# Optimization experiments

Measured on AMD Instinct MI355X. Metric: run time of the kernel, lower is better.

The kernel has to match this reference:

```python
import jax, jax.numpy as jnp
import numpy as np

B, S, D_IN, D_OUT = 4, 2048, 1024, 1024

def setup_inputs() -> dict:
    key = jax.random.key(0)
    k1, k2, k3, k4 = jax.random.split(key, 4)
    s = 0.02
    return {
        "X": jax.random.normal(k1, (B, S, D_IN), dtype=jnp.float32),
        "Wq": jax.random.normal(k2, (D_OUT, D_IN), dtype=jnp.float32) * s,
        "Wk": jax.random.normal(k3, (D_OUT, D_IN), dtype=jnp.float32) * s,
        "Wv": jax.random.normal(k4, (D_OUT, D_IN), dtype=jnp.float32) * s,
    }

def reference(X, Wq, Wk, Wv):
    # nn.Linear: y = x @ W.T (no bias)
    q = jnp.einsum('bsd,ed->bse', X, Wq)  # [B,S,D_OUT]
    k = jnp.einsum('bsd,ed->bse', X, Wk)
    v = jnp.einsum('bsd,ed->bse', X, Wv)
    scores = jnp.einsum('bqe,bke->bqk', q, k)  # [B,S,S]
    n = X.shape[1]
    causal = jnp.triu(jnp.ones((n, n), dtype=bool), k=1)
    scores = jnp.where(causal[None], -jnp.inf, scores)
    scale = 1.0 / jnp.sqrt(jnp.asarray(k.shape[-1], dtype=scores.dtype))
    attn = jax.nn.softmax(scores * scale, axis=-1)
    return jnp.einsum('bqk,bke->bqe', attn, v)
```

## Files before the change

kernel.cpp:

```cpp
#include <hip/hip_runtime.h>
#include <cstdint>


typedef __attribute__((ext_vector_type(8))) __bf16 bf16x8;
typedef __attribute__((ext_vector_type(4))) float f32x4;

#define BK 64

__device__ __forceinline__ unsigned short f2bf(float f) {
  union { float f; unsigned u; } v; v.f = f;
  unsigned r = v.u + 0x7fffu + ((v.u >> 16) & 1u);
  return (unsigned short)(r >> 16);
}

__device__ __forceinline__ void gload_lds16(const void* g, void* l) {
  __builtin_amdgcn_global_load_lds(
      (const __attribute__((address_space(1))) void*)g,
      (__attribute__((address_space(3))) void*)l, 16, 0, 0);
}

__global__ __launch_bounds__(256)
void cvt_all(const float* __restrict__ X, const float* __restrict__ Wq,
             const float* __restrict__ Wk, const float* __restrict__ Wv,
             unsigned short* __restrict__ Xbf, unsigned short* __restrict__ Wall,
             float* __restrict__ L) {
  const int bid = blockIdx.x;
  if (bid >= 11264) {
    float4* p = (float4*)(L + (size_t)(bid - 11264) * 2048);
    p[threadIdx.x] = (float4){0.f, 0.f, 0.f, 0.f};
    p[threadIdx.x + 256] = (float4){0.f, 0.f, 0.f, 0.f};
    return;
  }
  const float* src;
  unsigned short* dst;
  int i;
  if (bid < 8192) {
    src = X; dst = Xbf; i = bid * 256 + threadIdx.x;
  } else {
    const int m = bid - 8192;
    const int sel = m >> 10;
    src = (sel == 0) ? Wq : (sel == 1) ? Wk : Wv;
    dst = Wall + (size_t)sel * 1048576;
    i = (m & 1023) * 256 + threadIdx.x;
  }
  float4 v = ((const float4*)src)[i];
  ushort4 o;
  o.x = f2bf(v.x); o.y = f2bf(v.y); o.z = f2bf(v.z); o.w = f2bf(v.w);
  ((ushort4*)dst)[i] = o;
}

__global__ __launch_bounds__(256, 3)
void gemm_qkv(const unsigned short* __restrict__ A,
              const unsigned short* __restrict__ Bm,
              unsigned short* __restrict__ Qb,
              unsigned short* __restrict__ Kb,
              unsigned short* __restrict__ Vt,
              int bx0)
{
  const int NX = gridDim.x;
  const int lin = blockIdx.y * NX + blockIdx.x;
  const int chunk = (NX * 64) >> 3;
  const int swz = (lin & 7) * chunk + (lin >> 3);
  const int bx = swz % NX + bx0, by = swz / NX;

  __shared__ __align__(16) unsigned short As[128 * BK];
  __shared__ __align__(16) unsigned short Bs[128 * BK];

  const int tid = threadIdx.x;
  const int wave = tid >> 6, lane = tid & 63;
  const int wr = wave >> 1, wc = wave & 1;
  const int quad = lane >> 4, l16 = lane & 15;

  const unsigned rsub = wave * 8 + (lane >> 3);
  const unsigned csb = (unsigned)(((lane & 7) ^ ((lane >> 3) & 7)) * 16);

  unsigned offA[4], offB[4];
  #pragma unroll
  for (int s = 0; s < 4; ++s) {
    offA[s] = ((unsigned)(by * 128 + s * 32 + rsub) * 1024u) * 2u + csb;
    offB[s] = ((unsigned)(bx * 128 + s * 32 + rsub) * 1024u) * 2u + csb;
  }
  const char* Abase = (const char*)A;
  const char* Bbase = (const char*)Bm;

  f32x4 acc[4][4];
  #pragma unroll
  for (int i = 0; i < 4; ++i)
    #pragma unroll
    for (int j = 0; j < 4; ++j)
      acc[i][j] = (f32x4){0.f, 0.f, 0.f, 0.f};

  const int pq = (quad ^ (l16 & 7)) * 8;
  const int aOff = (wr * 64 + l16) * BK + pq;
  const int bOff = (wc * 64 + l16) * BK + pq;

  for (int k0 = 0; k0 < 1024; k0 += BK) {
    const unsigned kb = (unsigned)k0 * 2u;
    #pragma unroll
    for (int s = 0; s < 4; ++s) {
      gload_lds16(Abase + kb + offA[s], As + s * 2048 + wave * 512);
      gload_lds16(Bbase + kb + offB[s], Bs + s * 2048 + wave * 512);
    }
    __syncthreads();
    #pragma unroll
    for (int h = 0; h < 2; ++h) {
      const int hx = h * 32;
      bf16x8 af[4], bfr[4];
      #pragma unroll
      for (int i = 0; i < 4; ++i)
        af[i] = *(const bf16x8*)(As + ((aOff + i * 16 * BK) ^ hx));
      #pragma unroll
      for (int j = 0; j < 4; ++j)
        bfr[j] = *(const bf16x8*)(Bs + ((bOff + j * 16 * BK) ^ hx));
      #pragma unroll
      for (int i = 0; i < 4; ++i)
        #pragma unroll
        for (int j = 0; j < 4; ++j)
          acc[i][j] = __builtin_amdgcn_mfma_f32_16x16x32_bf16(af[i], bfr[j], acc[i][j], 0, 0, 0);
    }
    __syncthreads();
  }

  const int row0 = by * 128 + wr * 64 + quad * 4;
  const int col0 = bx * 128 + wc * 64 + l16;
  if (bx < 16) {
    unsigned short* C = (bx < 8) ? Qb : Kb;
    const int col = (bx < 8) ? col0 : col0 - 1024;
    #pragma unroll
    for (int i = 0; i < 4; ++i)
      #pragma unroll
      for (int r = 0; r < 4; ++r) {
        const size_t rr = (size_t)(row0 + i * 16 + r) * 1024;
        #pragma unroll
        for (int j = 0; j < 4; ++j)
          C[rr + col + j * 16] = f2bf(acc[i][j][r]);
      }
  } else {
    const int b = row0 >> 11;
    const int s0 = row0 & 2047;
    unsigned short* Vb = Vt + (size_t)b * 2097152;
    #pragma unroll
    for (int j = 0; j < 4; ++j) {
      const size_t ee = (size_t)(col0 - 2048 + j * 16) * 2048;
      #pragma unroll
      for (int i = 0; i < 4; ++i) {
        ushort4 o;
        o.x = f2bf(acc[i][j][0]); o.y = f2bf(acc[i][j][1]);
        o.z = f2bf(acc[i][j][2]); o.w = f2bf(acc[i][j][3]);
        *(ushort4*)(Vb + ee + s0 + i * 16) = o;
      }
    }
  }
}

__global__ __launch_bounds__(256, 3)
void gemm_scores(const unsigned short* __restrict__ Q,
                 const unsigned short* __restrict__ Km,
                 unsigned short* __restrict__ S,
                 float* __restrict__ L)
{
  const int t0i = blockIdx.x;
  const int t = (t0i & 7) * 17 + (t0i >> 3);
  const int bz = blockIdx.z;
  int by = (int)((sqrtf(8.f * t + 1.f) - 1.f) * 0.5f);
  while ((by + 1) * (by + 2) / 2 <= t) ++by;
  while (by * (by + 1) / 2 > t) --by;
  const int bx = t - by * (by + 1) / 2;

  __shared__ __align__(16) unsigned short As2[128 * BK];
  __shared__ __align__(16) unsigned short Bs2[128 * BK];

  const int tid = threadIdx.x;
  const int wave = tid >> 6, lane = tid & 63;
  const int wr = wave >> 1, wc = wave & 1;
  const int quad = lane >> 4, l16 = lane & 15;

  const unsigned rsub = wave * 8 + (lane >> 3);
  const unsigned csb = (unsigned)(((lane & 7) ^ ((lane >> 3) & 7)) * 16);

  unsigned offA[4], offB[4];
  #pragma unroll
  for (int s = 0; s < 4; ++s) {
    offA[s] = ((unsigned)(by * 128 + s * 32 + rsub) * 1024u) * 2u + csb;
    offB[s] = ((unsigned)(bx * 128 + s * 32 + rsub) * 1024u) * 2u + csb;
  }
  const char* Abase = (const char*)(Q + (size_t)bz * 2097152);
  const char* Bbase = (const char*)(Km + (size_t)bz * 2097152);

  f32x4 acc[4][4];
  #pragma unroll
  for (int i = 0; i < 4; ++i)
    #pragma unroll
    for (int j = 0; j < 4; ++j)
      acc[i][j] = (f32x4){0.f, 0.f, 0.f, 0.f};

  const int pq = (quad ^ (l16 & 7)) * 8;
  const int aOff = (wr * 64 + l16) * BK + pq;
  const int bOff = (wc * 64 + l16) * BK + pq;

  for (int k0 = 0; k0 < 1024; k0 += BK) {
    const unsigned kb = (unsigned)k0 * 2u;
    #pragma unroll
    for (int s = 0; s < 4; ++s) {
      gload_lds16(Abase + kb + offA[s], As2 + s * 2048 + wave * 512);
      gload_lds16(Bbase + kb + offB[s], Bs2 + s * 2048 + wave * 512);
    }
    __syncthreads();
    #pragma unroll
    for (int h = 0; h < 2; ++h) {
      const int hx = h * 32;
      bf16x8 af[4], bfr[4];
      #pragma unroll
      for (int i = 0; i < 4; ++i)
        af[i] = *(const bf16x8*)(As2 + ((aOff + i * 16 * BK) ^ hx));
      #pragma unroll
      for (int j = 0; j < 4; ++j)
        bfr[j] = *(const bf16x8*)(Bs2 + ((bOff + j * 16 * BK) ^ hx));
      #pragma unroll
      for (int i = 0; i < 4; ++i)
        #pragma unroll
        for (int j = 0; j < 4; ++j)
          acc[i][j] = __builtin_amdgcn_mfma_f32_16x16x32_bf16(af[i], bfr[j], acc[i][j], 0, 0, 0);
    }
    __syncthreads();
  }

  const int row0 = by * 128 + wr * 64 + quad * 4;
  const int col0 = bx * 128 + wc * 64 + l16;
  float* Lb = L + (size_t)bz * 2048;
  unsigned short* C = S + (size_t)bz * 4194304;

  #pragma unroll
  for (int i = 0; i < 4; ++i)
    #pragma unroll
    for (int r = 0; r < 4; ++r) {
      const int grow = row0 + i * 16 + r;
      float ps = 0.f;
      #pragma unroll
      for (int j = 0; j < 4; ++j) {
        const int gcol = col0 + j * 16;
        float e = (gcol <= grow) ? __expf(acc[i][j][r] * 0.03125f) : 0.f;
        acc[i][j][r] = e;
        ps += e;
      }
      #pragma unroll
      for (int m = 8; m > 0; m >>= 1)
        ps += __shfl_xor(ps, m);
      if (l16 == 0) atomicAdd(&Lb[grow], ps);
      const size_t rr = (size_t)grow * 2048;
      #pragma unroll
      for (int j = 0; j < 4; ++j)
        C[rr + col0 + j * 16] = f2bf(acc[i][j][r]);
    }
}

__global__ __launch_bounds__(256, 3)
void gemm_pv(const unsigned short* __restrict__ P,
             const unsigned short* __restrict__ Vt,
             float* __restrict__ Out,
             const float* __restrict__ L)
{
  const int bx = blockIdx.x, by = 15 - blockIdx.y, bz = blockIdx.z;

  __shared__ __align__(16) unsigned short As2[128 * BK];
  __shared__ __align__(16) unsigned short Bs2[128 * BK];

  const int tid = threadIdx.x;
  const int wave = tid >> 6, lane = tid & 63;
  const int wr = wave >> 1, wc = wave & 1;
  const int quad = lane >> 4, l16 = lane & 15;

  const unsigned rsub = wave * 8 + (lane >> 3);
  const unsigned csb = (unsigned)(((lane & 7) ^ ((lane >> 3) & 7)) * 16);

  unsigned offA[4], offB[4];
  #pragma unroll
  for (int s = 0; s < 4; ++s) {
    offA[s] = ((unsigned)(by * 128 + s * 32 + rsub) * 2048u) * 2u + csb;
    offB[s] = ((unsigned)(bx * 128 + s * 32 + rsub) * 2048u) * 2u + csb;
  }
  const char* Abase = (const char*)(P + (size_t)bz * 4194304);
  const char* Bbase = (const char*)(Vt + (size_t)bz * 2097152);

  f32x4 acc[4][4];
  #pragma unroll
  for (int i = 0; i < 4; ++i)
    #pragma unroll
    for (int j = 0; j < 4; ++j)
      acc[i][j] = (f32x4){0.f, 0.f, 0.f, 0.f};

  const int kmax = (by + 1) * 128;

  const int pq = (quad ^ (l16 & 7)) * 8;
  const int aOff = (wr * 64 + l16) * BK + pq;
  const int bOff = (wc * 64 + l16) * BK + pq;

  for (int k0 = 0; k0 < kmax; k0 += BK) {
    const unsigned kb = (unsigned)k0 * 2u;
    #pragma unroll
    for (int s = 0; s < 4; ++s) {
      gload_lds16(Abase + kb + offA[s], As2 + s * 2048 + wave * 512);
      gload_lds16(Bbase + kb + offB[s], Bs2 + s * 2048 + wave * 512);
    }
    __syncthreads();
    #pragma unroll
    for (int h = 0; h < 2; ++h) {
      const int hx = h * 32;
      bf16x8 af[4], bfr[4];
      #pragma unroll
      for (int i = 0; i < 4; ++i)
        af[i] = *(const bf16x8*)(As2 + ((aOff + i * 16 * BK) ^ hx));
      #pragma unroll
      for (int j = 0; j < 4; ++j)
        bfr[j] = *(const bf16x8*)(Bs2 + ((bOff + j * 16 * BK) ^ hx));
      #pragma unroll
      for (int i = 0; i < 4; ++i)
        #pragma unroll
        for (int j = 0; j < 4; ++j)
          acc[i][j] = __builtin_amdgcn_mfma_f32_16x16x32_bf16(af[i], bfr[j], acc[i][j], 0, 0, 0);
    }
    __syncthreads();
  }

  const int row0 = by * 128 + wr * 64 + quad * 4;
  const int col0 = bx * 128 + wc * 64 + l16;
  float* C = Out + (size_t)bz * 2097152;
  const float* Lb = L + (size_t)bz * 2048;
  #pragma unroll
  for (int i = 0; i < 4; ++i)
    #pragma unroll
    for (int r = 0; r < 4; ++r) {
      const int grow = row0 + i * 16 + r;
      const float inv = 1.0f / Lb[grow];
      const size_t rr = (size_t)grow * 1024;
      #pragma unroll
      for (int j = 0; j < 4; ++j)
        C[rr + col0 + j * 16] = acc[i][j][r] * inv;
    }
}

extern "C" void kernel_launch(void* const* d_in, const int* in_sizes, int n_in,
                              void* d_out, int out_size, void* d_ws, size_t ws_size,
                              hipStream_t stream) {
  const float* X  = (const float*)d_in[0];
  const float* Wq = (const float*)d_in[1];
  const float* Wk = (const float*)d_in[2];
  const float* Wv = (const float*)d_in[3];
  float* Out = (float*)d_out;

  char* ws = (char*)d_ws;
  unsigned short* Xbf  = (unsigned short*)(ws);
  unsigned short* Wall = (unsigned short*)(ws + 16777216);
  unsigned short* Qbf  = (unsigned short*)(ws + 23068672);
  unsigned short* Kbf  = (unsigned short*)(ws + 39845888);
  unsigned short* Vt   = (unsigned short*)(ws + 56623104);
  unsigned short* Sbf  = (unsigned short*)(ws + 73400320);
  float*          Lbuf = (float*)(ws + 106954752);

  cvt_all<<<11268, 256, 0, stream>>>(X, Wq, Wk, Wv, Xbf, Wall, Lbuf);

  gemm_qkv<<<dim3(16, 64), 256, 0, stream>>>(Xbf, Wall, Qbf, Kbf, Vt, 0);
  gemm_qkv<<<dim3(8, 64), 256, 0, stream>>>(Xbf, Wall, Qbf, Kbf, Vt, 16);

  gemm_scores<<<dim3(136, 1, 4), 256, 0, stream>>>(Qbf, Kbf, Sbf, Lbuf);

  gemm_pv<<<dim3(8, 16, 4), 256, 0, stream>>>(Sbf, Vt, Out, Lbuf);
}
```

Baseline: 223.2 us.

## Fuse V projection into scores kernel to share one launch

The V projection GEMM moves out of the separate second qkv launch into a combined kernel that also computes the causal scores tiles. Blocks are interleaved by index so V tiles and score tiles share the GPU, filling the tail of the triangular scores grid and removing one kernel launch. The cost is more complex block-index mapping and a heterogeneous grid whose tile mix may balance poorly.

```diff
diff --git a/kernel.cpp b/kernel.cpp
--- a/kernel.cpp
+++ b/kernel.cpp
@@ -53,15 +53,13 @@
 void gemm_qkv(const unsigned short* __restrict__ A,
               const unsigned short* __restrict__ Bm,
               unsigned short* __restrict__ Qb,
-              unsigned short* __restrict__ Kb,
-              unsigned short* __restrict__ Vt,
-              int bx0)
+              unsigned short* __restrict__ Kb)
 {
   const int NX = gridDim.x;
   const int lin = blockIdx.y * NX + blockIdx.x;
   const int chunk = (NX * 64) >> 3;
   const int swz = (lin & 7) * chunk + (lin >> 3);
-  const int bx = swz % NX + bx0, by = swz / NX;
+  const int bx = swz % NX, by = swz / NX;
 
   __shared__ __align__(16) unsigned short As[128 * BK];
   __shared__ __align__(16) unsigned short Bs[128 * BK];
@@ -123,25 +121,148 @@
 
   const int row0 = by * 128 + wr * 64 + quad * 4;
   const int col0 = bx * 128 + wc * 64 + l16;
-  if (bx < 16) {
-    unsigned short* C = (bx < 8) ? Qb : Kb;
-    const int col = (bx < 8) ? col0 : col0 - 1024;
+  unsigned short* C = (bx < 8) ? Qb : Kb;
+  const int col = (bx < 8) ? col0 : col0 - 1024;
+  #pragma unroll
+  for (int i = 0; i < 4; ++i)
+    #pragma unroll
+    for (int r = 0; r < 4; ++r) {
+      const size_t rr = (size_t)(row0 + i * 16 + r) * 1024;
+      #pragma unroll
+      for (int j = 0; j < 4; ++j)
+        C[rr + col + j * 16] = f2bf(acc[i][j][r]);
+    }
+}
+
+__global__ __launch_bounds__(256, 3)
+void gemm_sv(const unsigned short* __restrict__ Qb,
+             const unsigned short* __restrict__ Kb,
+             const unsigned short* __restrict__ Xbf,
+             const unsigned short* __restrict__ Wall,
+             unsigned short* __restrict__ S,
+             float* __restrict__ L,
+             unsigned short* __restrict__ Vt)
+{
+  const int lin = blockIdx.x;
+  const int c = lin & 7;
+  const int pos = lin >> 3;
+  const bool isV = (pos < 128) && (pos & 1);
+
+  int by, bxr, bz = 0;
+  const unsigned short *Ab, *Bb;
+  if (!isV) {
+    const int s_loc = (pos < 128) ? (pos >> 1) : (64 + (pos - 128));
+    const int sidx = c * 68 + s_loc;
+    bz = sidx / 136;
+    const int t = sidx - bz * 136;
+    int byy = (int)((sqrtf(8.f * t + 1.f) - 1.f) * 0.5f);
+    while ((byy + 1) * (byy + 2) / 2 <= t) ++byy;
+    while (byy * (byy + 1) / 2 > t) --byy;
+    by = byy;
+    bxr = t - byy * (byy + 1) / 2;
+    Ab = Qb + (size_t)bz * 2097152;
+    Bb = Kb + (size_t)bz * 2097152;
+  } else {
+    const int v = c * 64 + (pos >> 1);
+    by = v >> 3;
+    bxr = v & 7;
+    Ab = Xbf;
+    Bb = Wall + 2 * 1048576;
+  }
+
+  __shared__ __align__(16) unsigned short As2[128 * BK];
+  __shared__ __align__(16) unsigned short Bs2[128 * BK];
+
+  const int tid = threadIdx.x;
+  const int wave = tid >> 6, lane = tid & 63;
+  const int wr = wave >> 1, wc = wave & 1;
+  const int quad = lane >> 4, l16 = lane & 15;
+
+  const unsigned rsub = wave * 8 + (lane >> 3);
+  const unsigned csb = (unsigned)(((lane & 7) ^ ((lane >> 3) & 7)) * 16);
+
+  unsigned offA[4], offB[4];
+  #pragma unroll
+  for (int s = 0; s < 4; ++s) {
+    offA[s] = ((unsigned)(by * 128 + s * 32 + rsub) * 1024u) * 2u + csb;
+    offB[s] = ((unsigned)(bxr * 128 + s * 32 + rsub) * 1024u) * 2u + csb;
+  }
+  const char* Abase = (const char*)Ab;
+  const char* Bbase = (const char*)Bb;
+
+  f32x4 acc[4][4];
+  #pragma unroll
+  for (int i = 0; i < 4; ++i)
+    #pragma unroll
+    for (int j = 0; j < 4; ++j)
+      acc[i][j] = (f32x4){0.f, 0.f, 0.f, 0.f};
+
+  const int pq = (quad ^ (l16 & 7)) * 8;
+  const int aOff = (wr * 64 + l16) * BK + pq;
+  const int bOff = (wc * 64 + l16) * BK + pq;
+
+  for (int k0 = 0; k0 < 1024; k0 += BK) {
+    const unsigned kb = (unsigned)k0 * 2u;
+    #pragma unroll
+    for (int s = 0; s < 4; ++s) {
+      gload_lds16(Abase + kb + offA[s], As2 + s * 2048 + wave * 512);
+      gload_lds16(Bbase + kb + offB[s], Bs2 + s * 2048 + wave * 512);
+    }
+    __syncthreads();
+    #pragma unroll
+    for (int h = 0; h < 2; ++h) {
+      const int hx = h * 32;
+      bf16x8 af[4], bfr[4];
+      #pragma unroll
+      for (int i = 0; i < 4; ++i)
+        af[i] = *(const bf16x8*)(As2 + ((aOff + i * 16 * BK) ^ hx));
+      #pragma unroll
+      for (int j = 0; j < 4; ++j)
+        bfr[j] = *(const bf16x8*)(Bs2 + ((bOff + j * 16 * BK) ^ hx));
+      #pragma unroll
+      for (int i = 0; i < 4; ++i)
+        #pragma unroll
+        for (int j = 0; j < 4; ++j)
+          acc[i][j] = __builtin_amdgcn_mfma_f32_16x16x32_bf16(af[i], bfr[j], acc[i][j], 0, 0, 0);
+    }
+    __syncthreads();
+  }
+
+  const int row0 = by * 128 + wr * 64 + quad * 4;
+  if (!isV) {
+    const int col0 = bxr * 128 + wc * 64 + l16;
+    float* Lb = L + (size_t)bz * 2048;
+    unsigned short* C = S + (size_t)bz * 4194304;
     #pragma unroll
     for (int i = 0; i < 4; ++i)
       #pragma unroll
       for (int r = 0; r < 4; ++r) {
-        const size_t rr = (size_t)(row0 + i * 16 + r) * 1024;
+        const int grow = row0 + i * 16 + r;
+        float ps = 0.f;
+        #pragma unroll
+        for (int j = 0; j < 4; ++j) {
+          const int gcol = col0 + j * 16;
+          float e = (gcol <= grow) ? __expf(acc[i][j][r] * 0.03125f) : 0.f;
+          acc[i][j][r] = e;
+          ps += e;
+        }
+        #pragma unroll
+        for (int m = 8; m > 0; m >>= 1)
+          ps += __shfl_xor(ps, m);
+        if (l16 == 0) atomicAdd(&Lb[grow], ps);
+        const size_t rr = (size_t)grow * 2048;
         #pragma unroll
         for (int j = 0; j < 4; ++j)
-          C[rr + col + j * 16] = f2bf(acc[i][j][r]);
+          C[rr + col0 + j * 16] = f2bf(acc[i][j][r]);
       }
   } else {
     const int b = row0 >> 11;
     const int s0 = row0 & 2047;
     unsigned short* Vb = Vt + (size_t)b * 2097152;
+    const int e0 = bxr * 128 + wc * 64 + l16;
     #pragma unroll
     for (int j = 0; j < 4; ++j) {
-      const size_t ee = (size_t)(col0 - 2048 + j * 16) * 2048;
+      const size_t ee = (size_t)(e0 + j * 16) * 2048;
       #pragma unroll
       for (int i = 0; i < 4; ++i) {
         ushort4 o;
@@ -151,107 +272,6 @@
       }
     }
   }
-}
-
-__global__ __launch_bounds__(256, 3)
-void gemm_scores(const unsigned short* __restrict__ Q,
-                 const unsigned short* __restrict__ Km,
-                 unsigned short* __restrict__ S,
-                 float* __restrict__ L)
-{
-  const int t0i = blockIdx.x;
-  const int t = (t0i & 7) * 17 + (t0i >> 3);
-  const int bz = blockIdx.z;
-  int by = (int)((sqrtf(8.f * t + 1.f) - 1.f) * 0.5f);
-  while ((by + 1) * (by + 2) / 2 <= t) ++by;
-  while (by * (by + 1) / 2 > t) --by;
-  const int bx = t - by * (by + 1) / 2;
-
-  __shared__ __align__(16) unsigned short As2[128 * BK];
-  __shared__ __align__(16) unsigned short Bs2[128 * BK];
-
-  const int tid = threadIdx.x;
-  const int wave = tid >> 6, lane = tid & 63;
-  const int wr = wave >> 1, wc = wave & 1;
-  const int quad = lane >> 4, l16 = lane & 15;
-
-  const unsigned rsub = wave * 8 + (lane >> 3);
-  const unsigned csb = (unsigned)(((lane & 7) ^ ((lane >> 3) & 7)) * 16);
-
-  unsigned offA[4], offB[4];
-  #pragma unroll
-  for (int s = 0; s < 4; ++s) {
-    offA[s] = ((unsigned)(by * 128 + s * 32 + rsub) * 1024u) * 2u + csb;
-    offB[s] = ((unsigned)(bx * 128 + s * 32 + rsub) * 1024u) * 2u + csb;
-  }
-  const char* Abase = (const char*)(Q + (size_t)bz * 2097152);
-  const char* Bbase = (const char*)(Km + (size_t)bz * 2097152);
-
-  f32x4 acc[4][4];
-  #pragma unroll
-  for (int i = 0; i < 4; ++i)
-    #pragma unroll
-    for (int j = 0; j < 4; ++j)
-      acc[i][j] = (f32x4){0.f, 0.f, 0.f, 0.f};
-
-  const int pq = (quad ^ (l16 & 7)) * 8;
-  const int aOff = (wr * 64 + l16) * BK + pq;
-  const int bOff = (wc * 64 + l16) * BK + pq;
-
-  for (int k0 = 0; k0 < 1024; k0 += BK) {
-    const unsigned kb = (unsigned)k0 * 2u;
-    #pragma unroll
-    for (int s = 0; s < 4; ++s) {
-      gload_lds16(Abase + kb + offA[s], As2 + s * 2048 + wave * 512);
-      gload_lds16(Bbase + kb + offB[s], Bs2 + s * 2048 + wave * 512);
-    }
-    __syncthreads();
-    #pragma unroll
-    for (int h = 0; h < 2; ++h) {
-      const int hx = h * 32;
-      bf16x8 af[4], bfr[4];
-      #pragma unroll
-      for (int i = 0; i < 4; ++i)
-        af[i] = *(const bf16x8*)(As2 + ((aOff + i * 16 * BK) ^ hx));
-      #pragma unroll
-      for (int j = 0; j < 4; ++j)
-        bfr[j] = *(const bf16x8*)(Bs2 + ((bOff + j * 16 * BK) ^ hx));
-      #pragma unroll
-      for (int i = 0; i < 4; ++i)
-        #pragma unroll
-        for (int j = 0; j < 4; ++j)
-          acc[i][j] = __builtin_amdgcn_mfma_f32_16x16x32_bf16(af[i], bfr[j], acc[i][j], 0, 0, 0);
-    }
-    __syncthreads();
-  }
-
-  const int row0 = by * 128 + wr * 64 + quad * 4;
-  const int col0 = bx * 128 + wc * 64 + l16;
-  float* Lb = L + (size_t)bz * 2048;
-  unsigned short* C = S + (size_t)bz * 4194304;
-
-  #pragma unroll
-  for (int i = 0; i < 4; ++i)
-    #pragma unroll
-    for (int r = 0; r < 4; ++r) {
-      const int grow = row0 + i * 16 + r;
-      float ps = 0.f;
-      #pragma unroll
-      for (int j = 0; j < 4; ++j) {
-        const int gcol = col0 + j * 16;
-        float e = (gcol <= grow) ? __expf(acc[i][j][r] * 0.03125f) : 0.f;
-        acc[i][j][r] = e;
-        ps += e;
-      }
-      #pragma unroll
-      for (int m = 8; m > 0; m >>= 1)
-        ps += __shfl_xor(ps, m);
-      if (l16 == 0) atomicAdd(&Lb[grow], ps);
-      const size_t rr = (size_t)grow * 2048;
-      #pragma unroll
-      for (int j = 0; j < 4; ++j)
-        C[rr + col0 + j * 16] = f2bf(acc[i][j][r]);
-    }
 }
 
 __global__ __launch_bounds__(256, 3)
@@ -359,10 +379,9 @@
 
   cvt_all<<<11268, 256, 0, stream>>>(X, Wq, Wk, Wv, Xbf, Wall, Lbuf);
 
-  gemm_qkv<<<dim3(16, 64), 256, 0, stream>>>(Xbf, Wall, Qbf, Kbf, Vt, 0);
-  gemm_qkv<<<dim3(8, 64), 256, 0, stream>>>(Xbf, Wall, Qbf, Kbf, Vt, 16);
-
-  gemm_scores<<<dim3(136, 1, 4), 256, 0, stream>>>(Qbf, Kbf, Sbf, Lbuf);
+  gemm_qkv<<<dim3(16, 64), 256, 0, stream>>>(Xbf, Wall, Qbf, Kbf);
+
+  gemm_sv<<<1056, 256, 0, stream>>>(Qbf, Kbf, Xbf, Wall, Sbf, Lbuf, Vt);
 
   gemm_pv<<<dim3(8, 16, 4), 256, 0, stream>>>(Sbf, Vt, Out, Lbuf);
 }
```

Result: faster. 218.0 us (-2.3%).
